# Kernel tuning notes

Measured on AMD Instinct MI355X. Metric: run time of the kernel, lower is better.

## Reference

```python
import jax, jax.numpy as jnp
import numpy as np

B, S, D = 8, 2048, 512  # batch, seq_len, d_model (= units*heads = 64*8)


def setup_inputs() -> dict:
    key = jax.random.key(0)
    k1, k2, k3, k4 = jax.random.split(key, 4)
    scale = 1.0 / np.sqrt(D)
    return {
        "data": jax.random.normal(k1, (B, S, D), dtype=jnp.float32),
        "Wq": jax.random.normal(k2, (D, D), dtype=jnp.float32) * scale,
        "Wk": jax.random.normal(k3, (D, D), dtype=jnp.float32) * scale,
        "Wv": jax.random.normal(k4, (D, D), dtype=jnp.float32) * scale,
    }


def reference(data, Wq, Wk, Wv):
    # Bias-free projections (no head split in the original module).
    q = data @ Wq  # [B,S,D]
    k = data @ Wk
    v = data @ Wv
    scores = jnp.einsum("bsd,btd->bst", q, k)  # [B,S,S]
    # NOTE: original scales by sqrt(weight.shape[-1]) == sqrt(seq_len), not sqrt(d_k).
    scores = scores / jnp.sqrt(jnp.float32(scores.shape[-1]))
    # Causal mask: (w + 1e6) * tril - 1e6  ==  where(tril, w, -1e6)
    causal = jnp.tril(jnp.ones((scores.shape[1], scores.shape[2]), dtype=bool))
    scores = jnp.where(causal[None, :, :], scores, jnp.float32(-1e6))
    attn = jax.nn.softmax(scores, axis=-1)
    return jnp.einsum("bst,btd->bsd", attn, v)  # [B,S,D]
```

## Files before the change

kernel.cpp:

```cpp
#include <hip/hip_runtime.h>

typedef unsigned short u16;
typedef __attribute__((ext_vector_type(8))) short short8;
typedef __attribute__((ext_vector_type(4))) float f32x4;


__device__ __forceinline__ u16 f2bf(float f) {
    unsigned u = __float_as_uint(f);
    u += 0x7fffu + ((u >> 16) & 1u);
    return (u16)(u >> 16);
}

__device__ __forceinline__ void lds_cp16(const u16* g, u16* l) {
#if defined(__has_builtin) && __has_builtin(__builtin_amdgcn_global_load_lds)
    __builtin_amdgcn_global_load_lds(
        (const __attribute__((address_space(1))) void*)g,
        (__attribute__((address_space(3))) void*)l, 16, 0, 0);
#else
    *(uint4*)l = *(const uint4*)g;
#endif
}

template <bool ROWSUM>
__device__ __forceinline__ void gemm_core(const u16* __restrict__ Ag, int lda,
                                          const u16* __restrict__ Bg, int ldb,
                                          int ksteps, u16* Alds, u16* Blds,
                                          f32x4 (&acc)[4][4], f32x4* accL) {
    const int t = threadIdx.x;
    const int lane = t & 63;
    const int w = t >> 6;
    const int wr = (w >> 1) * 64;
    const int wc = (w & 1) * 64;
    const int el0 = t * 8;
    const short ob = (short)0x3f80;
    const short8 ones = {ob, ob, ob, ob, ob, ob, ob, ob};

    auto stage = [&](int kt, int buf) {
#pragma unroll
        for (int p = 0; p < 2; ++p) {
            const int el = el0 + p * 2048;
            const int row = el >> 5, col = el & 31;
            lds_cp16(Ag + (size_t)row * lda + kt * 32 + col, Alds + buf * 4096 + el);
            lds_cp16(Bg + (size_t)row * ldb + kt * 32 + col, Blds + buf * 4096 + el);
        }
    };

    stage(0, 0);
    int cur = 0;
    for (int kt = 0; kt < ksteps; ++kt) {
        __syncthreads();
        if (kt + 1 < ksteps) stage(kt + 1, cur ^ 1);
        const short8* A8 = (const short8*)(Alds + cur * 4096);
        const short8* B8 = (const short8*)(Blds + cur * 4096);
        short8 a[4], b[4];
#pragma unroll
        for (int i = 0; i < 4; ++i)
            a[i] = A8[(wr + i * 16 + (lane & 15)) * 4 + (lane >> 4)];
#pragma unroll
        for (int j = 0; j < 4; ++j)
            b[j] = B8[(wc + j * 16 + (lane & 15)) * 4 + (lane >> 4)];
#pragma unroll
        for (int i = 0; i < 4; ++i)
#pragma unroll
            for (int j = 0; j < 4; ++j)
                acc[i][j] = __builtin_amdgcn_mfma_f32_16x16x32_bf16(a[i], b[j], acc[i][j], 0, 0, 0);
        if constexpr (ROWSUM) {
#pragma unroll
            for (int i = 0; i < 4; ++i)
                accL[i] = __builtin_amdgcn_mfma_f32_16x16x32_bf16(a[i], ones, accL[i], 0, 0, 0);
        }
        cur ^= 1;
    }
}


__global__ void k_cvt_x(const float4* __restrict__ X, ushort4* __restrict__ Xb, int n4) {
    for (int i = blockIdx.x * blockDim.x + threadIdx.x; i < n4; i += gridDim.x * blockDim.x) {
        float4 v = X[i];
        ushort4 o;
        o.x = f2bf(v.x); o.y = f2bf(v.y); o.z = f2bf(v.z); o.w = f2bf(v.w);
        Xb[i] = o;
    }
}

__global__ void k_cvt_w(const float* __restrict__ Wq, const float* __restrict__ Wk,
                        const float* __restrict__ Wv, u16* __restrict__ Wt) {
    int idx = blockIdx.x * 256 + threadIdx.x;
    int z = idx >> 18;
    int nk = idx & 262143;
    int n = nk >> 9, k = nk & 511;
    const float* W = (z == 0) ? Wq : (z == 1 ? Wk : Wv);
    float v = W[k * 512 + n];
    if (z == 0) v *= 0.022097086912079608f;
    Wt[idx] = f2bf(v);
}

__global__ __launch_bounds__(256, 4) void k_proj(const u16* __restrict__ Xb, const u16* __restrict__ Wt,
                                                 u16* __restrict__ Qb, u16* __restrict__ Kb,
                                                 u16* __restrict__ Vt) {
    __shared__ alignas(16) u16 Alds[2][4096];
    __shared__ alignas(16) u16 Blds[2][4096];
    const int bid = blockIdx.x;
    const int u = bid >> 3;
    const int z = u >> 6;
    const int nt = (u >> 4) & 3;
    const int mt = (bid & 7) * 16 + (u & 15);
    const u16* Ag = Xb + (size_t)mt * 128 * 512;
    const u16* Bg = Wt + (size_t)z * 512 * 512 + (size_t)nt * 128 * 512;
    f32x4 acc[4][4] = {};
    gemm_core<false>(Ag, 512, Bg, 512, 16, &Alds[0][0], &Blds[0][0], acc, (f32x4*)nullptr);

    const int t = threadIdx.x, lane = t & 63, w = t >> 6;
    const int wr = (w >> 1) * 64, wc = (w & 1) * 64;
    if (z < 2) {
        u16* O = (z == 0) ? Qb : Kb;
#pragma unroll
        for (int i = 0; i < 4; ++i)
#pragma unroll
            for (int j = 0; j < 4; ++j)
#pragma unroll
                for (int r = 0; r < 4; ++r) {
                    int m = mt * 128 + wr + i * 16 + 4 * (lane >> 4) + r;
                    int n = nt * 128 + wc + j * 16 + (lane & 15);
                    O[(size_t)m * 512 + n] = f2bf(acc[i][j][r]);
                }
    } else {
        int b = mt >> 4;
#pragma unroll
        for (int i = 0; i < 4; ++i)
#pragma unroll
            for (int j = 0; j < 4; ++j) {
                int s0 = (mt * 128 + wr + i * 16 + 4 * (lane >> 4)) & 2047;
                int d = nt * 128 + wc + j * 16 + (lane & 15);
                ushort4 pk;
                pk.x = f2bf(acc[i][j][0]); pk.y = f2bf(acc[i][j][1]);
                pk.z = f2bf(acc[i][j][2]); pk.w = f2bf(acc[i][j][3]);
                *(ushort4*)(Vt + (size_t)b * 512 * 2048 + (size_t)d * 2048 + s0) = pk;
            }
    }
}

__global__ __launch_bounds__(256, 4) void k_scores(const u16* __restrict__ Qb, const u16* __restrict__ Kb,
                                                   u16* __restrict__ P) {
    const int bid = blockIdx.x;
    const int bz = bid & 7;
    const int tt = bid >> 3;
    int qi = (int)((sqrtf(8.0f * tt + 1.0f) - 1.0f) * 0.5f);
    while ((qi + 1) * (qi + 2) / 2 <= tt) ++qi;
    while (qi * (qi + 1) / 2 > tt) --qi;
    const int kvj = tt - qi * (qi + 1) / 2;

    __shared__ alignas(16) u16 Alds[2][4096];
    __shared__ alignas(16) u16 Blds[2][4096];
    const u16* Ag = Qb + (size_t)bz * 2048 * 512 + (size_t)qi * 128 * 512;
    const u16* Bg = Kb + (size_t)bz * 2048 * 512 + (size_t)kvj * 128 * 512;
    f32x4 acc[4][4] = {};
    gemm_core<false>(Ag, 512, Bg, 512, 16, &Alds[0][0], &Blds[0][0], acc, (f32x4*)nullptr);

    const int t = threadIdx.x, lane = t & 63, w = t >> 6;
    const int wr = (w >> 1) * 64, wc = (w & 1) * 64;
    u16* Pb = P + (size_t)bz * 2048 * 2048;
#pragma unroll
    for (int i = 0; i < 4; ++i)
#pragma unroll
        for (int j = 0; j < 4; ++j)
#pragma unroll
            for (int r = 0; r < 4; ++r) {
                int q = qi * 128 + wr + i * 16 + 4 * (lane >> 4) + r;
                int kv = kvj * 128 + wc + j * 16 + (lane & 15);
                float pv = (kv <= q) ? __expf(acc[i][j][r]) : 0.0f;
                Pb[(size_t)q * 2048 + kv] = f2bf(pv);
            }
}

__global__ __launch_bounds__(256, 4) void k_pv(const u16* __restrict__ P, const u16* __restrict__ Vt,
                                               float* __restrict__ Out) {
    __shared__ alignas(16) u16 Alds[2][2048];
    __shared__ alignas(16) u16 Blds[2][4096];
    const int bid = blockIdx.x;
    const int bz = bid & 7;
    const int u = bid >> 3;
    const int g = u >> 5;
    const int s = u & 31;
    const int nt = g;
    const int qi2 = (g & 1) ? (31 - s) : s;
    const int ksteps = (qi2 + 1) * 2;

    const int t = threadIdx.x, lane = t & 63, w = t >> 6;
    const int l = lane & 15, g4 = lane >> 4;
    const int wr = (w >> 1) * 32, wc = (w & 1) * 64;
    const u16* Ag = P + (size_t)bz * 2048 * 2048 + (size_t)qi2 * 64 * 2048;
    const u16* Bg = Vt + (size_t)bz * 512 * 2048 + (size_t)nt * 128 * 2048;
    const short ob = (short)0x3f80;
    const short8 ones = {ob, ob, ob, ob, ob, ob, ob, ob};

    auto stage = [&](int kt, int buf) {
        {
            const int el = t * 8;
            const int row = el >> 5, col = el & 31;
            lds_cp16(Ag + (size_t)row * 2048 + kt * 32 + col, &Alds[buf][el]);
        }
#pragma unroll
        for (int p = 0; p < 2; ++p) {
            const int el = t * 8 + p * 2048;
            const int row = el >> 5, col = el & 31;
            lds_cp16(Bg + (size_t)row * 2048 + kt * 32 + col, &Blds[buf][el]);
        }
    };

    f32x4 acc[2][4] = {};
    f32x4 accL[2] = {};
    stage(0, 0);
    int cur = 0;
    for (int kt = 0; kt < ksteps; ++kt) {
        __syncthreads();
        if (kt + 1 < ksteps) stage(kt + 1, cur ^ 1);
        const short8* A8 = (const short8*)&Alds[cur][0];
        const short8* B8 = (const short8*)&Blds[cur][0];
        short8 a[2], b[4];
#pragma unroll
        for (int i = 0; i < 2; ++i) a[i] = A8[(wr + i * 16 + l) * 4 + g4];
#pragma unroll
        for (int j = 0; j < 4; ++j) b[j] = B8[(wc + j * 16 + l) * 4 + g4];
#pragma unroll
        for (int i = 0; i < 2; ++i) {
#pragma unroll
            for (int j = 0; j < 4; ++j)
                acc[i][j] = __builtin_amdgcn_mfma_f32_16x16x32_bf16(a[i], b[j], acc[i][j], 0, 0, 0);
            accL[i] = __builtin_amdgcn_mfma_f32_16x16x32_bf16(a[i], ones, accL[i], 0, 0, 0);
        }
        cur ^= 1;
    }

#pragma unroll
    for (int i = 0; i < 2; ++i) {
        float inv[4];
#pragma unroll
        for (int r = 0; r < 4; ++r) inv[r] = 1.0f / accL[i][r];
#pragma unroll
        for (int j = 0; j < 4; ++j) {
            const int d = nt * 128 + wc + j * 16 + l;
#pragma unroll
            for (int r = 0; r < 4; ++r) {
                const int q = qi2 * 64 + wr + i * 16 + 4 * g4 + r;
                Out[(size_t)bz * 2048 * 512 + (size_t)q * 512 + d] = acc[i][j][r] * inv[r];
            }
        }
    }
}


extern "C" void kernel_launch(void* const* d_in, const int* in_sizes, int n_in,
                              void* d_out, int out_size, void* d_ws, size_t ws_size,
                              hipStream_t stream) {
    const float* data = (const float*)d_in[0];
    const float* Wq = (const float*)d_in[1];
    const float* Wk = (const float*)d_in[2];
    const float* Wv = (const float*)d_in[3];
    float* out = (float*)d_out;
    char* ws = (char*)d_ws;

    u16* Xb = (u16*)(ws);
    u16* Qb = (u16*)(ws + 16777216);
    u16* Kb = (u16*)(ws + 33554432);
    u16* Vt = (u16*)(ws + 50331648);
    u16* Wt = (u16*)(ws + 67108864);
    u16* P  = (u16*)(ws + 68681728);

    k_cvt_x<<<2048, 256, 0, stream>>>((const float4*)data, (ushort4*)Xb, (8 * 2048 * 512) / 4);
    k_cvt_w<<<3072, 256, 0, stream>>>(Wq, Wk, Wv, Wt);
    k_proj<<<1536, 256, 0, stream>>>(Xb, Wt, Qb, Kb, Vt);
    k_scores<<<1088, 256, 0, stream>>>(Qb, Kb, P);
    k_pv<<<1024, 256, 0, stream>>>(P, Vt, out);
}
```

Measured before the change: 131.7 us.

## Rewrite QKV projection as 256x256-tile, 8-wave pipelined GEMM

Replaces the 128x128 projection GEMM (1536 blocks of 256 threads) with a 256x256-tile kernel using 512 threads and 384 blocks. K is staged in half-slices into double-buffered, XOR-swizzled LDS, with prefetch interleaved between MFMA phases and explicit vmcnt waits. s_setprio is raised around MFMA bursts. The aim is better operand reuse per loaded byte and more overlap of global loads with compute. In exchange it uses more LDS and registers per block and leaves fewer blocks to spread across CUs.

```diff
diff --git a/kernel.cpp b/kernel.cpp
--- a/kernel.cpp
+++ b/kernel.cpp
@@ -19,6 +19,12 @@
 #else
     *(uint4*)l = *(const uint4*)g;
 #endif
+}
+
+__device__ __forceinline__ void bar() {
+    asm volatile("" ::: "memory");
+    __builtin_amdgcn_s_barrier();
+    asm volatile("" ::: "memory");
 }
 
 template <bool ROWSUM>
@@ -95,46 +101,131 @@
     Wt[idx] = f2bf(v);
 }
 
-__global__ __launch_bounds__(256, 4) void k_proj(const u16* __restrict__ Xb, const u16* __restrict__ Wt,
-                                                 u16* __restrict__ Qb, u16* __restrict__ Kb,
-                                                 u16* __restrict__ Vt) {
-    __shared__ alignas(16) u16 Alds[2][4096];
-    __shared__ alignas(16) u16 Blds[2][4096];
+__global__ __launch_bounds__(512, 2) void k_proj8(const u16* __restrict__ Xb, const u16* __restrict__ Wt,
+                                                  u16* __restrict__ Qb, u16* __restrict__ Kb,
+                                                  u16* __restrict__ Vt) {
+    __shared__ alignas(16) u16 LA[2][2][8192];
+    __shared__ alignas(16) u16 LB[2][2][8192];
     const int bid = blockIdx.x;
-    const int u = bid >> 3;
-    const int z = u >> 6;
-    const int nt = (u >> 4) & 3;
-    const int mt = (bid & 7) * 16 + (u & 15);
-    const u16* Ag = Xb + (size_t)mt * 128 * 512;
-    const u16* Bg = Wt + (size_t)z * 512 * 512 + (size_t)nt * 128 * 512;
-    f32x4 acc[4][4] = {};
-    gemm_core<false>(Ag, 512, Bg, 512, 16, &Alds[0][0], &Blds[0][0], acc, (f32x4*)nullptr);
-
-    const int t = threadIdx.x, lane = t & 63, w = t >> 6;
-    const int wr = (w >> 1) * 64, wc = (w & 1) * 64;
+    const int mt = (bid & 7) * 8 + ((bid >> 3) & 7);
+    const int ntl = bid >> 6;
+    const int t = threadIdx.x;
+    const int lane = t & 63, w = t >> 6;
+    const int l15 = lane & 15, g4 = lane >> 4;
+    const int wm = w >> 2, wn = w & 3;
+
+    const u16* Ag = Xb + (size_t)mt * 256 * 512;
+    const u16* Bg = Wt + (size_t)ntl * 256 * 512;
+
+    auto stageH = [&](const u16* gb, u16* lh, int kt, int ks) {
+#pragma unroll
+        for (int r = 0; r < 2; ++r) {
+            const int el = t * 8 + r * 4096;
+            const int R2 = el >> 6;
+            const int cl = ((el & 63) * 2) ^ ((R2 & 7) << 4);
+            const int row = R2 * 2 + (cl >> 6);
+            const int k = (cl & 63) >> 1;
+            lds_cp16(gb + (size_t)row * 512 + kt * 64 + ks * 32 + k, lh + el);
+        }
+    };
+    auto frag = [&](const u16* half, int row) -> short8 {
+        const int R2 = row >> 1;
+        const int c = (((row & 1) << 6) | (g4 << 4)) ^ ((R2 & 7) << 4);
+        return *(const short8*)(half + R2 * 64 + (c >> 1));
+    };
+
+    f32x4 acc[8][4] = {};
+
+    stageH(Bg, &LB[0][0][0], 0, 0);
+    stageH(Ag, &LA[0][0][0], 0, 0);
+    stageH(Bg, &LB[0][1][0], 0, 1);
+    stageH(Ag, &LA[0][1][0], 0, 1);
+    stageH(Bg, &LB[1][0][0], 1, 0);
+    stageH(Ag, &LA[1][0][0], 1, 0);
+    asm volatile("s_waitcnt vmcnt(8)" ::: "memory");
+    bar();
+
+#pragma unroll
+    for (int kt = 0; kt < 8; ++kt) {
+        const int bf = kt & 1;
+        short8 a[4], b[4];
+#pragma unroll
+        for (int nf = 0; nf < 4; ++nf) b[nf] = frag(&LB[bf][0][0], wn * 64 + nf * 16 + l15);
+#pragma unroll
+        for (int i = 0; i < 4; ++i) a[i] = frag(&LA[bf][0][0], wm * 128 + i * 16 + l15);
+        if (kt + 1 < 8) stageH(Bg, &LB[(kt + 1) & 1][1][0], kt + 1, 1);
+        bar();
+        __builtin_amdgcn_s_setprio(1);
+#pragma unroll
+        for (int i = 0; i < 4; ++i)
+#pragma unroll
+            for (int nf = 0; nf < 4; ++nf)
+                acc[i][nf] = __builtin_amdgcn_mfma_f32_16x16x32_bf16(a[i], b[nf], acc[i][nf], 0, 0, 0);
+        __builtin_amdgcn_s_setprio(0);
+#pragma unroll
+        for (int i = 0; i < 4; ++i) a[i] = frag(&LA[bf][0][0], wm * 128 + 64 + i * 16 + l15);
+        if (kt + 1 < 8) stageH(Ag, &LA[(kt + 1) & 1][1][0], kt + 1, 1);
+        if (kt < 7) asm volatile("s_waitcnt vmcnt(8)" ::: "memory");
+        else        asm volatile("s_waitcnt vmcnt(0)" ::: "memory");
+        bar();
+        __builtin_amdgcn_s_setprio(1);
+#pragma unroll
+        for (int i = 0; i < 4; ++i)
+#pragma unroll
+            for (int nf = 0; nf < 4; ++nf)
+                acc[4 + i][nf] = __builtin_amdgcn_mfma_f32_16x16x32_bf16(a[i], b[nf], acc[4 + i][nf], 0, 0, 0);
+        __builtin_amdgcn_s_setprio(0);
+#pragma unroll
+        for (int nf = 0; nf < 4; ++nf) b[nf] = frag(&LB[bf][1][0], wn * 64 + nf * 16 + l15);
+#pragma unroll
+        for (int i = 0; i < 4; ++i) a[i] = frag(&LA[bf][1][0], wm * 128 + i * 16 + l15);
+        if (kt + 2 < 8) stageH(Bg, &LB[kt & 1][0][0], kt + 2, 0);
+        bar();
+        __builtin_amdgcn_s_setprio(1);
+#pragma unroll
+        for (int i = 0; i < 4; ++i)
+#pragma unroll
+            for (int nf = 0; nf < 4; ++nf)
+                acc[i][nf] = __builtin_amdgcn_mfma_f32_16x16x32_bf16(a[i], b[nf], acc[i][nf], 0, 0, 0);
+        __builtin_amdgcn_s_setprio(0);
+#pragma unroll
+        for (int i = 0; i < 4; ++i) a[i] = frag(&LA[bf][1][0], wm * 128 + 64 + i * 16 + l15);
+        if (kt + 2 < 8) stageH(Ag, &LA[kt & 1][0][0], kt + 2, 0);
+        if (kt < 6)      asm volatile("s_waitcnt vmcnt(8)" ::: "memory");
+        else if (kt == 6) asm volatile("s_waitcnt vmcnt(4)" ::: "memory");
+        bar();
+        __builtin_amdgcn_s_setprio(1);
+#pragma unroll
+        for (int i = 0; i < 4; ++i)
+#pragma unroll
+            for (int nf = 0; nf < 4; ++nf)
+                acc[4 + i][nf] = __builtin_amdgcn_mfma_f32_16x16x32_bf16(a[i], b[nf], acc[4 + i][nf], 0, 0, 0);
+        __builtin_amdgcn_s_setprio(0);
+    }
+
+    const int z = ntl >> 1;
+    const int nc0 = (ntl & 1) * 256 + wn * 64;
+    const int m0 = mt * 256 + wm * 128;
     if (z < 2) {
         u16* O = (z == 0) ? Qb : Kb;
 #pragma unroll
-        for (int i = 0; i < 4; ++i)
-#pragma unroll
-            for (int j = 0; j < 4; ++j)
-#pragma unroll
-                for (int r = 0; r < 4; ++r) {
-                    int m = mt * 128 + wr + i * 16 + 4 * (lane >> 4) + r;
-                    int n = nt * 128 + wc + j * 16 + (lane & 15);
-                    O[(size_t)m * 512 + n] = f2bf(acc[i][j][r]);
-                }
+        for (int mf = 0; mf < 8; ++mf)
+#pragma unroll
+            for (int nf = 0; nf < 4; ++nf)
+#pragma unroll
+                for (int r = 0; r < 4; ++r)
+                    O[(size_t)(m0 + mf * 16 + 4 * g4 + r) * 512 + nc0 + nf * 16 + l15] = f2bf(acc[mf][nf][r]);
     } else {
-        int b = mt >> 4;
-#pragma unroll
-        for (int i = 0; i < 4; ++i)
-#pragma unroll
-            for (int j = 0; j < 4; ++j) {
-                int s0 = (mt * 128 + wr + i * 16 + 4 * (lane >> 4)) & 2047;
-                int d = nt * 128 + wc + j * 16 + (lane & 15);
+        const int b = mt >> 3;
+#pragma unroll
+        for (int mf = 0; mf < 8; ++mf)
+#pragma unroll
+            for (int nf = 0; nf < 4; ++nf) {
+                const int s0 = (mt & 7) * 256 + wm * 128 + mf * 16 + 4 * g4;
+                const int d = nc0 + nf * 16 + l15;
                 ushort4 pk;
-                pk.x = f2bf(acc[i][j][0]); pk.y = f2bf(acc[i][j][1]);
-                pk.z = f2bf(acc[i][j][2]); pk.w = f2bf(acc[i][j][3]);
+                pk.x = f2bf(acc[mf][nf][0]); pk.y = f2bf(acc[mf][nf][1]);
+                pk.z = f2bf(acc[mf][nf][2]); pk.w = f2bf(acc[mf][nf][3]);
                 *(ushort4*)(Vt + (size_t)b * 512 * 2048 + (size_t)d * 2048 + s0) = pk;
             }
     }
@@ -269,7 +360,7 @@
 
     k_cvt_x<<<2048, 256, 0, stream>>>((const float4*)data, (ushort4*)Xb, (8 * 2048 * 512) / 4);
     k_cvt_w<<<3072, 256, 0, stream>>>(Wq, Wk, Wv, Wt);
-    k_proj<<<1536, 256, 0, stream>>>(Xb, Wt, Qb, Kb, Vt);
+    k_proj8<<<384, 512, 0, stream>>>(Xb, Wt, Qb, Kb, Vt);
     k_scores<<<1088, 256, 0, stream>>>(Qb, Kb, P);
     k_pv<<<1024, 256, 0, stream>>>(P, Vt, out);
 }
```

Result: slower. 138.3 us (+5.0%).
